# Kernel optimization log

Measured on AMD Instinct MI355X. Metric: run time of the kernel, lower is better.

The kernel has to match this reference:

```python
import jax, jax.numpy as jnp
import numpy as np

N = 25000   # total nodes across the batch of graphs
K = 16      # sample_size_per_layer
H = 128     # encoder_hidden_dim
E = 128     # embedding_size
V = 32000   # vocab size
B = 50      # number of graphs / sql sequences
L = 128     # sql sequence length
NT = 4      # tokens per node name
NLAYERS = 3 # sample_layer_size


def _nrm(k, shape):
    return jax.random.normal(k, shape, dtype=jnp.float32) * 0.05


def setup_inputs() -> dict:
    key = jax.random.key(0)
    ks = iter(jax.random.split(key, 48))
    inp = {}
    inp["embed"] = _nrm(next(ks), (V, E))
    for d in ("seq_f", "seq_b", "node"):
        inp[d + "_Wih"] = _nrm(next(ks), (4 * H, E))
        inp[d + "_Whh"] = _nrm(next(ks), (4 * H, H))
        inp[d + "_b"] = _nrm(next(ks), (4 * H,))
    for d in ("fw", "bw"):
        inp[d + "_att0"] = _nrm(next(ks), (2, H))
        inp[d + "_attr"] = _nrm(next(ks), (NLAYERS - 1, 2, 2 * H))
        inp[d + "_Wg0"] = _nrm(next(ks), (H, H))
        inp[d + "_bg0"] = _nrm(next(ks), (H,))
        inp[d + "_Wgr"] = _nrm(next(ks), (NLAYERS - 1, 2 * H, 2 * H))
        inp[d + "_bgr"] = _nrm(next(ks), (NLAYERS - 1, 2 * H))
        inp[d + "_Wo0"] = _nrm(next(ks), (2, H, H))
        inp[d + "_bo0"] = _nrm(next(ks), (2, H))
        inp[d + "_Wor"] = _nrm(next(ks), (NLAYERS - 1, 2, 2 * H, H))
        inp[d + "_bor"] = _nrm(next(ks), (NLAYERS - 1, 2, H))
    inp["node_features"] = jax.random.randint(next(ks), (N, NT), 0, V)
    inp["fw_adj"] = jax.random.randint(next(ks), (N + 1, K), 0, N + 1)  # index N = zero-pad row
    inp["bw_adj"] = jax.random.randint(next(ks), (N + 1, K), 0, N + 1)
    inp["idx_sql_seqs"] = jax.random.randint(next(ks), (B, L), 0, V)
    lens = jax.random.randint(next(ks), (B,), 16, L + 1)
    inp["sql_seqs_lens"] = lens.at[0].set(L)  # ensure max(lens) == L like pad_packed
    inp["max_len"] = 1000  # nodes per graph (equal-size graphs)
    return inp


def _lstm(x, Wih, Whh, b):
    # x: [B, T, E] -> [B, T, H]; torch LSTM gate order i, f, g, o (bih+bhh folded into b)
    xg = jnp.einsum('bte,ge->btg', x, Wih) + b
    h0 = jnp.zeros((x.shape[0], Whh.shape[1]), x.dtype)
    def step(carry, gt):
        h, c = carry
        g = gt + h @ Whh.T
        i, f, gg, o = jnp.split(g, 4, axis=-1)
        c = jax.nn.sigmoid(f) * c + jax.nn.sigmoid(i) * jnp.tanh(gg)
        h = jax.nn.sigmoid(o) * jnp.tanh(c)
        return (h, c), h
    _, hs = jax.lax.scan(step, (h0, h0), jnp.swapaxes(xg, 0, 1))
    return jnp.swapaxes(hs, 0, 1)


def _gated_attn(self_h, neigh, att, Wg, bg, Wo, bo):
    # additive attention over K sampled neighbors, gated context, concat output (2*H)
    scores = jnp.einsum('nkd,d->nk', neigh, att[1]) + (self_h @ att[0])[:, None]
    a = jax.nn.softmax(scores, axis=-1)
    ctx = jnp.einsum('nk,nkd->nd', a, neigh)
    gate = jax.nn.sigmoid(self_h @ Wg + bg)
    from_self = jax.nn.relu(self_h @ Wo[0] + bo[0])
    from_neigh = jax.nn.relu((gate * ctx) @ Wo[1] + bo[1])
    return jnp.concatenate([from_self, from_neigh], axis=-1)


def reference(embed, seq_f_Wih, seq_f_Whh, seq_f_b, seq_b_Wih, seq_b_Whh, seq_b_b,
              node_Wih, node_Whh, node_b,
              fw_att0, fw_attr, fw_Wg0, fw_bg0, fw_Wgr, fw_bgr, fw_Wo0, fw_bo0, fw_Wor, fw_bor,
              bw_att0, bw_attr, bw_Wg0, bw_bg0, bw_Wgr, bw_bgr, bw_Wo0, bw_bo0, bw_Wor, bw_bor,
              node_features, fw_adj, bw_adj, idx_sql_seqs, sql_seqs_lens, max_len):
    Bq, Lq = idx_sql_seqs.shape
    # --- SQL sequence encoder: bi-LSTM with length-aware reverse (pack/pad semantics) ---
    se = embed[idx_sql_seqs]                              # [B, L, E]
    fwd = _lstm(se, seq_f_Wih, seq_f_Whh, seq_f_b)
    rev_idx = jnp.clip(sql_seqs_lens[:, None] - 1 - jnp.arange(Lq)[None, :], 0, Lq - 1)
    se_rev = jnp.take_along_axis(se, rev_idx[..., None], 1)
    bwd = jnp.take_along_axis(_lstm(se_rev, seq_b_Wih, seq_b_Whh, seq_b_b), rev_idx[..., None], 1)
    valid = (jnp.arange(Lq)[None, :] < sql_seqs_lens[:, None])[..., None]
    seqs_encoding = jnp.concatenate([fwd, bwd], -1) * valid  # padded positions zeroed
    seqs_encoding_mask = (idx_sql_seqs == 0)
    # --- node feature encoder: last hidden of a uni-LSTM over node tokens ---
    node_embedding = _lstm(embed[node_features], node_Wih, node_Whh, node_b)[:, -1, :]  # [N, H]
    fw_nbrs = fw_adj[:-1]  # [N, K]
    bw_nbrs = bw_adj[:-1]
    fw_hidden = node_embedding
    bw_hidden = node_embedding
    for l in range(NLAYERS):
        pad = jnp.zeros((1, fw_hidden.shape[1]), fw_hidden.dtype)
        fn = jnp.concatenate([fw_hidden, pad], 0)[fw_nbrs]  # [N, K, d]
        if l == 0:
            fw_hidden = _gated_attn(fw_hidden, fn, fw_att0, fw_Wg0, fw_bg0, fw_Wo0, fw_bo0)
        else:
            j = l - 1
            fw_hidden = _gated_attn(fw_hidden, fn, fw_attr[j], fw_Wgr[j], fw_bgr[j], fw_Wor[j], fw_bor[j])
        bn_ = jnp.concatenate([bw_hidden, pad], 0)[bw_nbrs]
        if l == 0:
            bw_hidden = _gated_attn(bw_hidden, bn_, bw_att0, bw_Wg0, bw_bg0, bw_Wo0, bw_bo0)
        else:
            j = l - 1
            bw_hidden = _gated_attn(bw_hidden, bn_, bw_attr[j], bw_Wgr[j], bw_bgr[j], bw_Wor[j], bw_bor[j])
    hidden = jax.nn.relu(jnp.concatenate([fw_hidden, bw_hidden], -1))  # [N, 4H]
    graph_hidden = hidden.reshape(hidden.shape[0] // max_len, max_len, hidden.shape[1])
    graph_embedding = graph_hidden.max(axis=1)
    return (graph_hidden, graph_embedding, max_len, seqs_encoding, seqs_encoding_mask)
```

## Files before the change

### kernel.cpp

```cpp
#include <hip/hip_runtime.h>
#include <math.h>

#define NN 25000
#define KNB 16
#define HH 128
#define VV 32000
#define BB 50
#define LL 128
#define NTK 4
#define NGRAPH 25
#define GCH 20

typedef __attribute__((ext_vector_type(8))) short s16x8;
typedef __attribute__((ext_vector_type(4))) float f32x4;
typedef _Float16 h16x2 __attribute__((ext_vector_type(2)));

__device__ __forceinline__ float fexp2(float x) {
#if __has_builtin(__builtin_amdgcn_exp2f)
    return __builtin_amdgcn_exp2f(x);
#else
    return exp2f(x);
#endif
}
__device__ __forceinline__ float frcp(float x) {
#if __has_builtin(__builtin_amdgcn_rcpf)
    return __builtin_amdgcn_rcpf(x);
#else
    return 1.f / x;
#endif
}
__device__ __forceinline__ float fsigm(float x) { return frcp(1.f + fexp2(x * -1.4426950408889634f)); }
__device__ __forceinline__ float ftanh(float x) { return 1.f - 2.f * frcp(1.f + fexp2(x * 2.8853900817779268f)); }

__device__ __forceinline__ unsigned short f2bf(float x) {
    unsigned int u = __float_as_uint(x);
    unsigned int r = (u + 0x7fffu + ((u >> 16) & 1u)) >> 16;
    return (unsigned short)r;
}
__device__ __forceinline__ float bf2f(unsigned int b) {
    return __uint_as_float((b & 0xffffu) << 16);
}

template<int CTRL>
__device__ __forceinline__ float qxor(float x) {
#if __has_builtin(__builtin_amdgcn_mov_dpp)
    return __int_as_float(__builtin_amdgcn_mov_dpp(__float_as_int(x), CTRL, 0xf, 0xf, true));
#else
    int m = (CTRL == 0xB1) ? 1 : (CTRL == 0x4E) ? 2 : 3;
    return __shfl_xor(x, m, 64);
#endif
}

__device__ __forceinline__ float hdot(unsigned int a, unsigned int b, float c) {
#if __has_builtin(__builtin_amdgcn_fdot2)
    return __builtin_amdgcn_fdot2(__builtin_bit_cast(h16x2, a), __builtin_bit_cast(h16x2, b), c, false);
#else
    h16x2 av = __builtin_bit_cast(h16x2, a), bv = __builtin_bit_cast(h16x2, b);
    return c + (float)av[0] * (float)bv[0] + (float)av[1] * (float)bv[1];
#endif
}

__global__ __launch_bounds__(256) void embconv_k(const float* __restrict__ e,
                                                 unsigned short* __restrict__ o)
{
    int i = blockIdx.x * 256 + threadIdx.x;
    if (i < VV * 128) o[i] = f2bf(e[i]);
}

__global__ __launch_bounds__(256) void wprep_k(
    const float* __restrict__ ndWih, const float* __restrict__ ndWhh,
    const float* __restrict__ fWg0, const float* __restrict__ fWgr,
    const float* __restrict__ fWo0, const float* __restrict__ fWor,
    const float* __restrict__ bWg0, const float* __restrict__ bWgr,
    const float* __restrict__ bWo0, const float* __restrict__ bWor,
    const float* __restrict__ sfWih, const float* __restrict__ sbWih,
    const float* __restrict__ sfWhh, const float* __restrict__ sbWhh,
    unsigned short* __restrict__ dst)
{
    int idx = blockIdx.x * 256 + threadIdx.x;
    if (idx >= 1146880) return;
    if (idx >= 884736) {
        int r = idx - 884736;
        int d = r >> 17;
        int o = r & 131071;
        int pairIdx = o >> 1, hf = o & 1;
        int k2 = pairIdx >> 9, n = pairIdx & 511;
        int k = k2 * 2 + hf;
        int unit = n >> 2, gate = n & 3;
        const float* W = d ? sbWhh : sfWhh;
        _Float16 hv = (_Float16)W[(gate * 128 + unit) * 128 + k];
        dst[idx] = __builtin_bit_cast(unsigned short, hv);
        return;
    }
    float val;
    if (idx < 131072) {
        int r = idx >> 8, k = idx & 255;
        int unit = r >> 2, gate = r & 3;
        int srow = (gate << 7) + unit;
        val = (k < 128) ? ndWih[srow * 128 + k] : ndWhh[srow * 128 + (k - 128)];
    } else if (idx < 753664) {
        int r = idx - 131072;
        int dir = r / 311296;
        int o = r % 311296;
        const float* Wg0 = dir ? bWg0 : fWg0;
        const float* Wgr = dir ? bWgr : fWgr;
        const float* Wo0 = dir ? bWo0 : fWo0;
        const float* Wor = dir ? bWor : fWor;
        if (o < 16384) {
            int n = o >> 7, k = o & 127;
            val = Wg0[k * 128 + n];
        } else if (o < 147456) {
            int p = o - 16384;
            int j = p >> 16, q = p & 65535;
            int n = q >> 8, k = q & 255;
            val = Wgr[j * 65536 + k * 256 + n];
        } else if (o < 180224) {
            int p = o - 147456;
            int s = p >> 14, q = p & 16383;
            int n = q >> 7, k = q & 127;
            val = Wo0[s * 16384 + k * 128 + n];
        } else {
            int p = o - 180224;
            int js = p >> 15, q = p & 32767;
            int n = q >> 8, k = q & 255;
            val = Wor[js * 32768 + k * 128 + n];
        }
    } else if (idx < 819200) {
        val = sfWih[idx - 753664];
    } else {
        val = sbWih[idx - 819200];
    }
    dst[idx] = f2bf(val);
}

__global__ __launch_bounds__(256) void tokrev_k(const int* __restrict__ idx,
                                                const int* __restrict__ lens,
                                                int* __restrict__ tokrev)
{
    int t = blockIdx.x * 256 + threadIdx.x;
    if (t >= BB * LL) return;
    int b = t / LL, tt = t % LL;
    int r = lens[b] - 1 - tt;
    r = r < 0 ? 0 : (r > LL - 1 ? LL - 1 : r);
    tokrev[t] = idx[b * LL + r];
}

__global__ __launch_bounds__(256) void hgemm1_k(
    const unsigned short* __restrict__ embedbf,
    const int* __restrict__ gidxA, const int* __restrict__ gidxB,
    const unsigned short* __restrict__ WtA, const unsigned short* __restrict__ WtB,
    const float* __restrict__ biasA, const float* __restrict__ biasB,
    float* __restrict__ outA, float* __restrict__ outB)
{
    __shared__ unsigned short Asm[128 * 64];
    __shared__ unsigned short Bsm[128 * 64];
    const int tid = threadIdx.x;
    const int lane = tid & 63, w = tid >> 6;
    const int wm = w >> 1, wn = w & 1;
    const int lane15 = lane & 15, hi = lane >> 4;
    const int y = blockIdx.y;
    const int* gidx = (y < 4) ? gidxA : gidxB;
    const unsigned short* Wt = (y < 4) ? WtA : WtB;
    const float* bias = (y < 4) ? biasA : biasB;
    float* outp = (y < 4) ? outA : outB;
    const int bm0 = blockIdx.x * 128, bn0 = (y & 3) * 128;
    const int M = BB * LL, K = 128;
    f32x4 acc[4][4];
#pragma unroll
    for (int i = 0; i < 4; ++i)
#pragma unroll
        for (int j = 0; j < 4; ++j) acc[i][j] = (f32x4){0.f, 0.f, 0.f, 0.f};

    for (int kt = 0; kt < K; kt += 64) {
#pragma unroll
        for (int r = 0; r < 4; ++r) {
            int id = tid + r * 256;
            int row = id >> 3, cc = id & 7;
            int m = bm0 + row;
            s16x8 v = {0, 0, 0, 0, 0, 0, 0, 0};
            if (m < M) {
                int g = gidx[m];
                v = *(const s16x8*)(embedbf + (size_t)g * 128 + kt + cc * 8);
            }
            int byt = (cc * 16) ^ ((row & 7) << 4);
            *(s16x8*)((char*)Asm + row * 128 + byt) = v;
        }
#pragma unroll
        for (int r = 0; r < 4; ++r) {
            int id = tid + r * 256;
            int row = id >> 3, cc = id & 7;
            s16x8 v = *(const s16x8*)(Wt + (size_t)(bn0 + row) * K + kt + cc * 8);
            int byt = (cc * 16) ^ ((row & 7) << 4);
            *(s16x8*)((char*)Bsm + row * 128 + byt) = v;
        }
        __syncthreads();
#pragma unroll
        for (int ks = 0; ks < 2; ++ks) {
            s16x8 af[4], bf[4];
#pragma unroll
            for (int mi = 0; mi < 4; ++mi) {
                int row = wm * 64 + mi * 16 + lane15;
                int byt = (ks * 64 + (hi * 16)) ^ ((row & 7) << 4);
                af[mi] = *(const s16x8*)((char*)Asm + row * 128 + byt);
            }
#pragma unroll
            for (int ni = 0; ni < 4; ++ni) {
                int row = wn * 64 + ni * 16 + lane15;
                int byt = (ks * 64 + (hi * 16)) ^ ((row & 7) << 4);
                bf[ni] = *(const s16x8*)((char*)Bsm + row * 128 + byt);
            }
#pragma unroll
            for (int mi = 0; mi < 4; ++mi)
#pragma unroll
                for (int ni = 0; ni < 4; ++ni)
                    acc[mi][ni] = __builtin_amdgcn_mfma_f32_16x16x32_bf16(af[mi], bf[ni], acc[mi][ni], 0, 0, 0);
        }
        __syncthreads();
    }
#pragma unroll
    for (int mi = 0; mi < 4; ++mi) {
#pragma unroll
        for (int ni = 0; ni < 4; ++ni) {
            int n = bn0 + wn * 64 + ni * 16 + lane15;
#pragma unroll
            for (int j = 0; j < 4; ++j) {
                int m = bm0 + wm * 64 + mi * 16 + hi * 4 + j;
                if (m < M) {
                    float v = acc[mi][ni][j] + bias[n];
                    int nn = ((n & 127) << 2) | (n >> 7);
                    outp[(size_t)m * 512 + nn] = v;
                }
            }
        }
    }
}

__global__ __launch_bounds__(512, 4) void node_seq_k(
    const unsigned short* __restrict__ embedbf,
    const int* __restrict__ nodefeat,
    const unsigned short* __restrict__ hrd,
    const unsigned short* __restrict__ nodeW,
    const float* __restrict__ ndb,
    unsigned short* __restrict__ hwr,
    unsigned short* __restrict__ cbuf,
    int step,
    const float* __restrict__ xgf, const float* __restrict__ xgb,
    const unsigned short* __restrict__ wseq,
    const int* __restrict__ lens,
    float* __restrict__ senc,
    unsigned short* __restrict__ hseq, float* __restrict__ cseq)
{
    __shared__ __align__(16) unsigned char smem[32768 + 512];
    const int bid = blockIdx.x;
    const int tid = threadIdx.x;

    if (bid >= 784) {
        int sid = bid - 784;
        int dir = sid >= BB ? 1 : 0;
        int b = dir ? sid - BB : sid;
        int len = lens[b];
        int t0 = step * 32;
        if (t0 >= len) return;
        int t1 = t0 + 32 < len ? t0 + 32 : len;
        const float* xg = (dir ? xgb : xgf) + (size_t)b * LL * 512;
        const unsigned int* wp = (const unsigned int*)(wseq + dir * 131072);
        int q = tid & 3, unit = tid >> 2;
        unsigned int wreg[64];
#pragma unroll
        for (int k2 = 0; k2 < 64; ++k2) wreg[k2] = wp[k2 * 512 + tid];
        unsigned short* hlsq = (unsigned short*)smem;
        float cj = 0.f;
        if (step == 0) {
            if (tid < 128) hlsq[tid] = 0;
        } else {
            if (tid < 128) hlsq[tid] = hseq[sid * 128 + tid];
            if (q == 0) cj = cseq[sid * 128 + unit];
        }
        __syncthreads();
        float xcur = xg[(size_t)t0 * 512 + tid];
        int pb = 0;
        for (int t = t0; t < t1; ++t) {
            float xnext = (t + 1 < t1) ? xg[(size_t)(t + 1) * 512 + tid] : 0.f;
            const uint4* hp = (const uint4*)&hlsq[pb * 128];
            float p0 = 0.f, p1 = 0.f, p2 = 0.f, p3 = 0.f;
#pragma unroll
            for (int i = 0; i < 4; ++i) {
                uint4 h0 = hp[i * 4 + 0], h1 = hp[i * 4 + 1], h2 = hp[i * 4 + 2], h3 = hp[i * 4 + 3];
                const unsigned int* w0 = &wreg[i * 16];
                p0 = hdot(h0.x, w0[0], p0);  p0 = hdot(h0.y, w0[1], p0);
                p0 = hdot(h0.z, w0[2], p0);  p0 = hdot(h0.w, w0[3], p0);
                p1 = hdot(h1.x, w0[4], p1);  p1 = hdot(h1.y, w0[5], p1);
                p1 = hdot(h1.z, w0[6], p1);  p1 = hdot(h1.w, w0[7], p1);
                p2 = hdot(h2.x, w0[8], p2);  p2 = hdot(h2.y, w0[9], p2);
                p2 = hdot(h2.z, w0[10], p2); p2 = hdot(h2.w, w0[11], p2);
                p3 = hdot(h3.x, w0[12], p3); p3 = hdot(h3.y, w0[13], p3);
                p3 = hdot(h3.z, w0[14], p3); p3 = hdot(h3.w, w0[15], p3);
            }
            float accv = xcur + ((p0 + p1) + (p2 + p3));
            float tv = (q == 2) ? ftanh(accv) : fsigm(accv);
            float v1 = __shfl_xor(tv, 1), v2 = __shfl_xor(tv, 2), v3 = __shfl_xor(tv, 3);
            if (q == 0) {
                cj = v1 * cj + tv * v2;
                float hv = v3 * ftanh(cj);
                _Float16 hh = (_Float16)hv;
                hlsq[(pb ^ 1) * 128 + unit] = __builtin_bit_cast(unsigned short, hh);
                int tout = dir ? (len - 1 - t) : t;
                senc[((size_t)b * LL + tout) * 256 + dir * 128 + unit] = hv;
            }
            __syncthreads();
            pb ^= 1;
            xcur = xnext;
        }
        if (q == 0) cseq[sid * 128 + unit] = cj;
        if (tid < 128) hseq[sid * 128 + tid] = hlsq[pb * 128 + tid];
        return;
    }

    unsigned short* Asm = (unsigned short*)smem;
    unsigned short* Bsm = (unsigned short*)(smem + 16384);
    const int lane = tid & 63, w = tid >> 6;
    const int wm = w & 1, wn = w >> 1;
    const int lane15 = lane & 15, hi = lane >> 4, q = lane & 3;
    const int bx = bid % 196, y = bid / 196;
    const int bm0 = bx * 128, bn0 = y * 128;
    const int czero = (step == 0);

    f32x4 acc[4][2];
#pragma unroll
    for (int i = 0; i < 4; ++i)
#pragma unroll
        for (int j = 0; j < 2; ++j) acc[i][j] = (f32x4){0.f, 0.f, 0.f, 0.f};

    for (int kt = 0; kt < 256; kt += 64) {
#pragma unroll
        for (int r = 0; r < 2; ++r) {
            int id = tid + r * 512;
            int row = id >> 3, cc = id & 7;
            int m = bm0 + row;
            s16x8 v = {0, 0, 0, 0, 0, 0, 0, 0};
            if (m < NN) {
                int k0 = kt + cc * 8;
                if (k0 < 128) {
                    int g = nodefeat[m * NTK + step];
                    v = *(const s16x8*)(embedbf + (size_t)g * 128 + k0);
                } else if (!czero) {
                    v = *(const s16x8*)(hrd + (size_t)m * 128 + (k0 - 128));
                }
            }
            int byt = (cc * 16) ^ ((row & 7) << 4);
            *(s16x8*)((char*)Asm + row * 128 + byt) = v;
        }
#pragma unroll
        for (int r = 0; r < 2; ++r) {
            int id = tid + r * 512;
            int row = id >> 3, cc = id & 7;
            s16x8 v = *(const s16x8*)(nodeW + (size_t)(bn0 + row) * 256 + kt + cc * 8);
            int byt = (cc * 16) ^ ((row & 7) << 4);
            *(s16x8*)((char*)Bsm + row * 128 + byt) = v;
        }
        __syncthreads();
#pragma unroll
        for (int ks = 0; ks < 2; ++ks) {
            s16x8 af[4], bf[2];
#pragma unroll
            for (int mi = 0; mi < 4; ++mi) {
                int row = wm * 64 + mi * 16 + lane15;
                int byt = (ks * 64 + (hi * 16)) ^ ((row & 7) << 4);
                af[mi] = *(const s16x8*)((char*)Asm + row * 128 + byt);
            }
#pragma unroll
            for (int ni = 0; ni < 2; ++ni) {
                int row = wn * 32 + ni * 16 + lane15;
                int byt = (ks * 64 + (hi * 16)) ^ ((row & 7) << 4);
                bf[ni] = *(const s16x8*)((char*)Bsm + row * 128 + byt);
            }
#pragma unroll
            for (int mi = 0; mi < 4; ++mi)
#pragma unroll
                for (int ni = 0; ni < 2; ++ni)
                    acc[mi][ni] = __builtin_amdgcn_mfma_f32_16x16x32_bf16(af[mi], bf[ni], acc[mi][ni], 0, 0, 0);
        }
        __syncthreads();
    }
    unsigned short* cb = cbuf + (((size_t)bid * 8 + w) * 64 + lane) * 8;
    float crv[8];
    if (czero) {
#pragma unroll
        for (int i = 0; i < 8; ++i) crv[i] = 0.f;
    } else {
        uint4 w0 = *(const uint4*)cb;
        unsigned int wd[4] = {w0.x, w0.y, w0.z, w0.w};
#pragma unroll
        for (int i = 0; i < 8; ++i) crv[i] = bf2f(wd[i >> 1] >> ((i & 1) * 16));
    }
    const bool qb0 = (lane & 1), qb1 = (lane & 2);
#pragma unroll
    for (int mi = 0; mi < 4; ++mi) {
#pragma unroll
        for (int ni = 0; ni < 2; ++ni) {
            int n = bn0 + wn * 32 + ni * 16 + lane15;
            int unit = n >> 2;
            float bval = ndb[((n & 3) << 7) + unit];
#pragma unroll
            for (int j = 0; j < 4; ++j) {
                float v = acc[mi][ni][j] + bval;
                float tv = (q == 2) ? ftanh(v) : fsigm(v);
                float v1 = qxor<0xB1>(tv), v2 = qxor<0x4E>(tv), v3 = qxor<0x1B>(tv);
                if (q == j) {
                    float gf = qb0 ? (qb1 ? v2 : tv) : (qb1 ? v3 : v1);
                    float gig = qb0 ? (v1 * v3) : (tv * v2);
                    float go = qb0 ? (qb1 ? tv : v2) : (qb1 ? v1 : v3);
                    float cc = gf * crv[mi * 2 + ni] + gig;
                    crv[mi * 2 + ni] = cc;
                    int m = bm0 + wm * 64 + mi * 16 + hi * 4 + j;
                    if (m < NN) hwr[(size_t)m * HH + unit] = f2bf(go * ftanh(cc));
                }
            }
        }
    }
    unsigned int wd[4];
#pragma unroll
    for (int p = 0; p < 4; ++p)
        wd[p] = (unsigned int)f2bf(crv[2 * p]) | ((unsigned int)f2bf(crv[2 * p + 1]) << 16);
    *(uint4*)cb = make_uint4(wd[0], wd[1], wd[2], wd[3]);
}

template<int D, int OF32OUT>
__global__ __launch_bounds__(512, 1) void layer_fused_k(
    const unsigned short* __restrict__ cur, int curds,
    const unsigned short* __restrict__ ctx, int ctxds,
    const unsigned short* __restrict__ wg, int wgds,
    const float* __restrict__ bgf, const float* __restrict__ bgb,
    const unsigned short* __restrict__ wo, int wods, int wrs,
    const float* __restrict__ bof, const float* __restrict__ bob,
    void* __restrict__ outb, int outds)
{
    __shared__ unsigned short As[128 * D];
    __shared__ unsigned short Gs[128 * D];
    __shared__ unsigned short Ws[128 * 64];
    constexpr int gt = D / 128;
    const int tid = threadIdx.x;
    const int lane = tid & 63, w = tid >> 6;
    const int wm = w & 1, wn = w >> 1;
    const int lane15 = lane & 15, hi = lane >> 4;
    const int orig = blockIdx.x;
    const int work = (orig & 7) * 49 + (orig >> 3);
    const int dir = work / 196;
    const int mt = work % 196;
    const int bm0 = mt * 128;
    const unsigned short* curd = cur + (size_t)dir * curds;
    const unsigned short* ctxd = ctx + (size_t)dir * ctxds;
    const float* bg = dir ? bgb : bgf;
    const float* bo = dir ? bob : bof;

    constexpr int CH = D / 8;
#pragma unroll
    for (int r = 0; r < D / 32; ++r) {
        int id = tid + r * 512;
        int row = id / CH, cc = id % CH;
        int m = bm0 + row;
        s16x8 v = {0, 0, 0, 0, 0, 0, 0, 0};
        if (m < NN) v = *(const s16x8*)(curd + (size_t)m * D + cc * 8);
        *(s16x8*)((char*)As + row * (D * 2) + ((cc * 16) ^ ((row & 7) << 4))) = v;
    }
    __syncthreads();

#pragma unroll
    for (int p = 0; p <= gt; ++p) {
        const bool isgate = p < gt;
        const int colBase = isgate ? p * 128 : 0;
        const unsigned short* Wt = isgate ? (wg + (size_t)dir * wgds + (size_t)colBase * D)
                                          : (wo + (size_t)dir * wods);
        f32x4 acc[4][2];
#pragma unroll
        for (int i = 0; i < 4; ++i)
#pragma unroll
            for (int j = 0; j < 2; ++j) acc[i][j] = (f32x4){0.f, 0.f, 0.f, 0.f};
        for (int kt = 0; kt < D; kt += 64) {
#pragma unroll
            for (int r = 0; r < 2; ++r) {
                int id = tid + r * 512;
                int row = id >> 3, cc = id & 7;
                s16x8 v = *(const s16x8*)(Wt + (size_t)row * D + kt + cc * 8);
                *(s16x8*)((char*)Ws + row * 128 + ((cc * 16) ^ ((row & 7) << 4))) = v;
            }
            __syncthreads();
#pragma unroll
            for (int ks = 0; ks < 2; ++ks) {
                s16x8 af[4], bf[2];
#pragma unroll
                for (int mi = 0; mi < 4; ++mi) {
                    int row = wm * 64 + mi * 16 + lane15;
                    af[mi] = *(const s16x8*)((char*)As + row * (D * 2)
                              + (((kt + ks * 32 + hi * 8) * 2) ^ ((row & 7) << 4)));
                }
#pragma unroll
                for (int ni = 0; ni < 2; ++ni) {
                    int row = wn * 32 + ni * 16 + lane15;
                    bf[ni] = *(const s16x8*)((char*)Ws + row * 128
                              + (((ks * 32 + hi * 8) * 2) ^ ((row & 7) << 4)));
                }
#pragma unroll
                for (int mi = 0; mi < 4; ++mi)
#pragma unroll
                    for (int ni = 0; ni < 2; ++ni)
                        acc[mi][ni] = __builtin_amdgcn_mfma_f32_16x16x32_bf16(af[mi], bf[ni], acc[mi][ni], 0, 0, 0);
            }
            __syncthreads();
        }
#pragma unroll
        for (int mi = 0; mi < 4; ++mi) {
#pragma unroll
            for (int ni = 0; ni < 2; ++ni) {
                int ncol = wn * 32 + ni * 16 + lane15;
#pragma unroll
                for (int j = 0; j < 4; ++j) {
                    int rr = wm * 64 + mi * 16 + hi * 4 + j;
                    int m = bm0 + rr;
                    if (isgate) {
                        int col = colBase + ncol;
                        float v = acc[mi][ni][j] + bg[col];
                        int ma = (m < NN) ? m : 0;
                        v = fsigm(v) * bf2f(ctxd[(size_t)ma * D + col]);
                        *(unsigned short*)((char*)Gs + rr * (D * 2) + ((col * 2) ^ ((rr & 7) << 4))) = f2bf(v);
                    } else if (m < NN) {
                        float v = fmaxf(acc[mi][ni][j] + bo[ncol], 0.f);
                        if (OF32OUT) ((float*)outb)[(size_t)m * 512 + dir * 256 + ncol] = v;
                        else ((unsigned short*)outb)[(size_t)dir * outds + (size_t)m * 256 + ncol] = f2bf(v);
                    }
                }
            }
        }
    }
    __syncthreads();

    {
        const unsigned short* Wt = wo + (size_t)dir * wods + (size_t)wrs;
        f32x4 acc[4][2];
#pragma unroll
        for (int i = 0; i < 4; ++i)
#pragma unroll
            for (int j = 0; j < 2; ++j) acc[i][j] = (f32x4){0.f, 0.f, 0.f, 0.f};
        for (int kt = 0; kt < D; kt += 64) {
#pragma unroll
            for (int r = 0; r < 2; ++r) {
                int id = tid + r * 512;
                int row = id >> 3, cc = id & 7;
                s16x8 v = *(const s16x8*)(Wt + (size_t)row * D + kt + cc * 8);
                *(s16x8*)((char*)Ws + row * 128 + ((cc * 16) ^ ((row & 7) << 4))) = v;
            }
            __syncthreads();
#pragma unroll
            for (int ks = 0; ks < 2; ++ks) {
                s16x8 af[4], bf[2];
#pragma unroll
                for (int mi = 0; mi < 4; ++mi) {
                    int row = wm * 64 + mi * 16 + lane15;
                    af[mi] = *(const s16x8*)((char*)Gs + row * (D * 2)
                              + (((kt + ks * 32 + hi * 8) * 2) ^ ((row & 7) << 4)));
                }
#pragma unroll
                for (int ni = 0; ni < 2; ++ni) {
                    int row = wn * 32 + ni * 16 + lane15;
                    bf[ni] = *(const s16x8*)((char*)Ws + row * 128
                              + (((ks * 32 + hi * 8) * 2) ^ ((row & 7) << 4)));
                }
#pragma unroll
                for (int mi = 0; mi < 4; ++mi)
#pragma unroll
                    for (int ni = 0; ni < 2; ++ni)
                        acc[mi][ni] = __builtin_amdgcn_mfma_f32_16x16x32_bf16(af[mi], bf[ni], acc[mi][ni], 0, 0, 0);
            }
            __syncthreads();
        }
#pragma unroll
        for (int mi = 0; mi < 4; ++mi) {
#pragma unroll
            for (int ni = 0; ni < 2; ++ni) {
                int ncol = wn * 32 + ni * 16 + lane15;
#pragma unroll
                for (int j = 0; j < 4; ++j) {
                    int m = bm0 + wm * 64 + mi * 16 + hi * 4 + j;
                    if (m < NN) {
                        float v = fmaxf(acc[mi][ni][j] + bo[128 + ncol], 0.f);
                        if (OF32OUT) ((float*)outb)[(size_t)m * 512 + dir * 256 + 128 + ncol] = v;
                        else ((unsigned short*)outb)[(size_t)dir * outds + (size_t)m * 256 + 128 + ncol] = f2bf(v);
                    }
                }
            }
        }
    }
}

__global__ __launch_bounds__(256) void finalize_k(const int* __restrict__ idx,
                                                  const int* __restrict__ lens,
                                                  float* __restrict__ senc,
                                                  float* __restrict__ mask,
                                                  float* __restrict__ omax,
                                                  const int* __restrict__ mlin)
{
    int id = blockIdx.x * 256 + threadIdx.x;
    if (id == 0) omax[0] = (float)mlin[0];
    if (id >= BB * LL * 64) return;
    int row = id >> 6, c = id & 63;
    int b = row / LL, tt = row % LL;
    if (c == 0) mask[row] = (idx[row] == 0) ? 1.f : 0.f;
    if (tt >= lens[b]) *(float4*)&senc[(size_t)row * 256 + c * 4] = make_float4(0.f, 0.f, 0.f, 0.f);
}

template<int D>
__global__ __launch_bounds__(256) void sdot_k(const unsigned short* __restrict__ hidb, int hidds,
                                              const float* __restrict__ a1f, const float* __restrict__ a1b,
                                              float* __restrict__ s1)
{
    constexpr int V = D / 64;
    int dir = blockIdx.y;
    const unsigned short* hid = hidb + (size_t)dir * hidds;
    const float* att1 = dir ? a1b : a1f;
    int lane = threadIdx.x & 63, wid = threadIdx.x >> 6;
    int n = blockIdx.x * 4 + wid;
    if (n >= NN) return;
    float p = 0.f;
    if (V == 2) {
        unsigned int u = *(const unsigned int*)(hid + (size_t)n * D + lane * 2);
        p = bf2f(u) * att1[lane * 2] + bf2f(u >> 16) * att1[lane * 2 + 1];
    } else {
        uint2 u = *(const uint2*)(hid + (size_t)n * D + lane * 4);
        p = bf2f(u.x) * att1[lane * 4] + bf2f(u.x >> 16) * att1[lane * 4 + 1]
          + bf2f(u.y) * att1[lane * 4 + 2] + bf2f(u.y >> 16) * att1[lane * 4 + 3];
    }
#pragma unroll
    for (int m = 1; m < 64; m <<= 1) p += __shfl_xor(p, m);
    if (lane == 0) s1[dir * NN + n] = p;
}

template<int D>
__global__ __launch_bounds__(256) void attn_ctx3_k(const unsigned short* __restrict__ hidb, int hidds,
                                                   const int* __restrict__ adj0, const int* __restrict__ adj1,
                                                   const float* __restrict__ s1,
                                                   unsigned short* __restrict__ ctxb, int ctxds)
{
    constexpr int V = D / 64;
    int dir = blockIdx.y;
    const unsigned short* hid = hidb + (size_t)dir * hidds;
    const int* adj = dir ? adj1 : adj0;
    unsigned short* ctx = ctxb + (size_t)dir * ctxds;
    int lane = threadIdx.x & 63, wid = threadIdx.x >> 6;
    int n = blockIdx.x * 4 + wid;
    if (n >= NN) return;
    int nb[KNB];
    float sc[KNB];
#pragma unroll
    for (int k = 0; k < KNB; ++k) nb[k] = adj[n * KNB + k];
#pragma unroll
    for (int k = 0; k < KNB; ++k) sc[k] = (nb[k] < NN) ? s1[dir * NN + nb[k]] : 0.f;
    float mx = sc[0];
#pragma unroll
    for (int k = 1; k < KNB; ++k) mx = fmaxf(mx, sc[k]);
    float s = 0.f;
#pragma unroll
    for (int k = 0; k < KNB; ++k) { sc[k] = fexp2((sc[k] - mx) * 1.4426950408889634f); s += sc[k]; }
    float inv = frcp(s);
    float accv[V];
#pragma unroll
    for (int j = 0; j < V; ++j) accv[j] = 0.f;
#pragma unroll
    for (int k = 0; k < KNB; ++k) {
        if (nb[k] < NN) {
            if (V == 2) {
                unsigned int u = *(const unsigned int*)(hid + (size_t)nb[k] * D + lane * 2);
                accv[0] += sc[k] * bf2f(u);
                accv[1] += sc[k] * bf2f(u >> 16);
            } else {
                uint2 u = *(const uint2*)(hid + (size_t)nb[k] * D + lane * 4);
                accv[0] += sc[k] * bf2f(u.x);
                accv[1] += sc[k] * bf2f(u.x >> 16);
                accv[2] += sc[k] * bf2f(u.y);
                accv[3] += sc[k] * bf2f(u.y >> 16);
            }
        }
    }
#pragma unroll
    for (int j2 = 0; j2 < V; j2 += 2) {
        unsigned int pk = (unsigned int)f2bf(accv[j2] * inv) | ((unsigned int)f2bf(accv[j2 + 1] * inv) << 16);
        *(unsigned int*)(ctx + (size_t)n * D + lane * V + j2) = pk;
    }
}

__global__ __launch_bounds__(512) void gmax1_k(const float* __restrict__ gh, float* __restrict__ part)
{
    int g = blockIdx.x, ch = blockIdx.y;
    int c = threadIdx.x;
    const float* p = gh + ((size_t)g * 1000 + ch * (1000 / GCH)) * 512 + c;
    float m = -1e30f;
#pragma unroll 5
    for (int i = 0; i < 1000 / GCH; ++i) m = fmaxf(m, p[(size_t)i * 512]);
    part[((size_t)g * GCH + ch) * 512 + c] = m;
}

__global__ __launch_bounds__(512) void gmax2_k(const float* __restrict__ part, float* __restrict__ ge)
{
    int g = blockIdx.x;
    int c = threadIdx.x;
    float m = -1e30f;
#pragma unroll
    for (int i = 0; i < GCH; ++i) m = fmaxf(m, part[((size_t)g * GCH + i) * 512 + c]);
    ge[g * 512 + c] = m;
}

extern "C" void kernel_launch(void* const* d_in, const int* in_sizes, int n_in,
                              void* d_out, int out_size, void* d_ws, size_t ws_size,
                              hipStream_t stream)
{
    const float* embed = (const float*)d_in[0];
    const float* sfWhh = (const float*)d_in[2];
    const float* sfb   = (const float*)d_in[3];
    const float* sbWhh = (const float*)d_in[5];
    const float* sbb   = (const float*)d_in[6];
    const float* ndWih = (const float*)d_in[7];
    const float* ndWhh = (const float*)d_in[8];
    const float* ndb   = (const float*)d_in[9];
    const int* nodefeat = (const int*)d_in[30];
    const int* adj0     = (const int*)d_in[31];
    const int* adj1     = (const int*)d_in[32];
    const int* idxseq   = (const int*)d_in[33];
    const int* lens     = (const int*)d_in[34];
    const int* mlin     = (const int*)d_in[35];

    float* ws = (float*)d_ws;
    unsigned short* warena  = (unsigned short*)ws;
    unsigned short* embedbf = (unsigned short*)(ws + 573440);
    float* xgf = ws + 2621440;
    float* xgb = ws + 5898240;
    int*   tokrev = (int*)(ws + 9175040);
    unsigned short* hbf  = (unsigned short*)(ws + 9181440);
    unsigned short* hbf2 = (unsigned short*)(ws + 10781440);
    unsigned short* cbuf = (unsigned short*)(ws + 12381440);
    unsigned short* HA   = (unsigned short*)(ws + 573440);
    unsigned short* HB   = (unsigned short*)(ws + 6973440);
    unsigned short* ctxb = (unsigned short*)(ws + 13987072);
    float* s1buf = ws + 20387072;
    unsigned short* hseq = (unsigned short*)(ws + 20437072);
    float* cseq = ws + 20449872;
    float* gmaxp = ws + 573440;

    float* outf  = (float*)d_out;
    float* gh    = outf;
    float* ge    = outf + 12800000;
    float* omax  = outf + 12812800;
    float* senc  = outf + 12812801;
    float* omask = outf + 14451201;

    tokrev_k<<<dim3((BB * LL + 255) / 256), dim3(256), 0, stream>>>(idxseq, lens, tokrev);
    embconv_k<<<dim3(VV * 128 / 256), dim3(256), 0, stream>>>(embed, embedbf);
    wprep_k<<<dim3(4480), dim3(256), 0, stream>>>(ndWih, ndWhh,
        (const float*)d_in[12], (const float*)d_in[14], (const float*)d_in[16], (const float*)d_in[18],
        (const float*)d_in[22], (const float*)d_in[24], (const float*)d_in[26], (const float*)d_in[28],
        (const float*)d_in[1], (const float*)d_in[4], sfWhh, sbWhh, warena);

    hgemm1_k<<<dim3(50, 8), dim3(256), 0, stream>>>(embedbf, idxseq, tokrev,
        warena + 753664, warena + 819200, sfb, sbb, xgf, xgb);

    for (int t = 0; t < NTK; ++t) {
        const unsigned short* hrd = (t & 1) ? hbf2 : hbf;
        unsigned short* hwr = (t & 1) ? hbf : hbf2;
        node_seq_k<<<dim3(884), dim3(512), 0, stream>>>(embedbf, nodefeat, hrd,
            warena, ndb, hwr, cbuf, t,
            xgf, xgb, warena + 884736, lens, senc, hseq, cseq);
    }
    finalize_k<<<dim3(1600), dim3(256), 0, stream>>>(idxseq, lens, senc, omask, omax, mlin);

    for (int l = 0; l < 3; ++l) {
        int D = (l == 0) ? 128 : 256;
        int j = l - 1;
        const unsigned short* curb = (l == 0) ? hbf : (l == 1 ? HA : HB);
        int curds = (l == 0) ? 0 : NN * 256;
        int ctxds = NN * D;
        const float* a1f = (l == 0) ? (const float*)d_in[10] + 128 : (const float*)d_in[11] + (size_t)j * 512 + 256;
        const float* a1b = (l == 0) ? (const float*)d_in[20] + 128 : (const float*)d_in[21] + (size_t)j * 512 + 256;

        if (D == 128) {
            sdot_k<128><<<dim3(NN / 4, 2), dim3(256), 0, stream>>>(curb, curds, a1f, a1b, s1buf);
            attn_ctx3_k<128><<<dim3(NN / 4, 2), dim3(256), 0, stream>>>(curb, curds, adj0, adj1, s1buf, ctxb, ctxds);
        } else {
            sdot_k<256><<<dim3(NN / 4, 2), dim3(256), 0, stream>>>(curb, curds, a1f, a1b, s1buf);
            attn_ctx3_k<256><<<dim3(NN / 4, 2), dim3(256), 0, stream>>>(curb, curds, adj0, adj1, s1buf, ctxb, ctxds);
        }

        const unsigned short* wgb = warena + 131072 + ((l == 0) ? 0 : 16384 + j * 65536);
        const float* bgf = (l == 0) ? (const float*)d_in[13] : (const float*)d_in[15] + (size_t)j * 256;
        const float* bgb = (l == 0) ? (const float*)d_in[23] : (const float*)d_in[25] + (size_t)j * 256;
        const unsigned short* wob = warena + 131072 + ((l == 0) ? 147456 : 180224 + j * 65536);
        int wrs = (l == 0) ? 16384 : 32768;
        const float* bof = (l == 0) ? (const float*)d_in[17] : (const float*)d_in[19] + (size_t)j * 256;
        const float* bob = (l == 0) ? (const float*)d_in[27] : (const float*)d_in[29] + (size_t)j * 256;
        int outds = NN * 256;

        if (l == 0) {
            layer_fused_k<128, 0><<<dim3(392), dim3(512), 0, stream>>>(curb, curds, ctxb, ctxds,
                wgb, 311296, bgf, bgb, wob, 311296, wrs, bof, bob, HA, outds);
        } else if (l == 1) {
            layer_fused_k<256, 0><<<dim3(392), dim3(512), 0, stream>>>(curb, curds, ctxb, ctxds,
                wgb, 311296, bgf, bgb, wob, 311296, wrs, bof, bob, HB, outds);
        } else {
            layer_fused_k<256, 1><<<dim3(392), dim3(512), 0, stream>>>(curb, curds, ctxb, ctxds,
                wgb, 311296, bgf, bgb, wob, 311296, wrs, bof, bob, gh, 0);
        }
    }

    gmax1_k<<<dim3(NGRAPH, GCH), dim3(512), 0, stream>>>(gh, gmaxp);
    gmax2_k<<<dim3(NGRAPH), dim3(512), 0, stream>>>(gmaxp, ge);
}
```

Before: 606.2 us.

## Halve layer GEMM row tile to 64 and double blocks for occupancy

The fused gated-attention layer kernel now processes 64 rows per block instead of 128, halving its shared-memory footprint and doubling the grid to 784 blocks, with launch bounds raised to allow two blocks per CU. Each wave now computes a 16x64 output strip (one A fragment, four B fragments) instead of 64x32. The gate results are packed in pairs via lane shuffles into 32-bit LDS writes. This aims to improve occupancy and load balance across CUs, but weight tiles are reloaded twice as often per output row and each A fragment is reused less.

```diff
diff --git a/kernel.cpp b/kernel.cpp
--- a/kernel.cpp
+++ b/kernel.cpp
@@ -426,7 +426,7 @@
 }
 
 template<int D, int OF32OUT>
-__global__ __launch_bounds__(512, 1) void layer_fused_k(
+__global__ __launch_bounds__(512, 2) void layer_fused_k(
     const unsigned short* __restrict__ cur, int curds,
     const unsigned short* __restrict__ ctx, int ctxds,
     const unsigned short* __restrict__ wg, int wgds,
@@ -435,19 +435,19 @@
     const float* __restrict__ bof, const float* __restrict__ bob,
     void* __restrict__ outb, int outds)
 {
-    __shared__ unsigned short As[128 * D];
-    __shared__ unsigned short Gs[128 * D];
+    __shared__ unsigned short As[64 * D];
+    __shared__ unsigned short Gs[64 * D];
     __shared__ unsigned short Ws[128 * 64];
     constexpr int gt = D / 128;
     const int tid = threadIdx.x;
     const int lane = tid & 63, w = tid >> 6;
-    const int wm = w & 1, wn = w >> 1;
+    const int wm = w >> 1, wn = w & 1;
     const int lane15 = lane & 15, hi = lane >> 4;
     const int orig = blockIdx.x;
-    const int work = (orig & 7) * 49 + (orig >> 3);
-    const int dir = work / 196;
-    const int mt = work % 196;
-    const int bm0 = mt * 128;
+    const int work = (orig & 7) * 98 + (orig >> 3);
+    const int dir = work / 392;
+    const int mt = work % 392;
+    const int bm0 = mt * 64;
     const unsigned short* curd = cur + (size_t)dir * curds;
     const unsigned short* ctxd = ctx + (size_t)dir * ctxds;
     const float* bg = dir ? bgb : bgf;
@@ -455,7 +455,7 @@
 
     constexpr int CH = D / 8;
 #pragma unroll
-    for (int r = 0; r < D / 32; ++r) {
+    for (int r = 0; r < D / 64; ++r) {
         int id = tid + r * 512;
         int row = id / CH, cc = id % CH;
         int m = bm0 + row;
@@ -471,11 +471,9 @@
         const int colBase = isgate ? p * 128 : 0;
         const unsigned short* Wt = isgate ? (wg + (size_t)dir * wgds + (size_t)colBase * D)
                                           : (wo + (size_t)dir * wods);
-        f32x4 acc[4][2];
-#pragma unroll
-        for (int i = 0; i < 4; ++i)
-#pragma unroll
-            for (int j = 0; j < 2; ++j) acc[i][j] = (f32x4){0.f, 0.f, 0.f, 0.f};
+        f32x4 acc[4];
+#pragma unroll
+        for (int i = 0; i < 4; ++i) acc[i] = (f32x4){0.f, 0.f, 0.f, 0.f};
         for (int kt = 0; kt < D; kt += 64) {
 #pragma unroll
             for (int r = 0; r < 2; ++r) {
@@ -487,47 +485,44 @@
             __syncthreads();
 #pragma unroll
             for (int ks = 0; ks < 2; ++ks) {
-                s16x8 af[4], bf[2];
-#pragma unroll
-                for (int mi = 0; mi < 4; ++mi) {
-                    int row = wm * 64 + mi * 16 + lane15;
-                    af[mi] = *(const s16x8*)((char*)As + row * (D * 2)
+                s16x8 af;
+                {
+                    int row = wm * 16 + lane15;
+                    af = *(const s16x8*)((char*)As + row * (D * 2)
                               + (((kt + ks * 32 + hi * 8) * 2) ^ ((row & 7) << 4)));
                 }
 #pragma unroll
-                for (int ni = 0; ni < 2; ++ni) {
-                    int row = wn * 32 + ni * 16 + lane15;
-                    bf[ni] = *(const s16x8*)((char*)Ws + row * 128
+                for (int ni = 0; ni < 4; ++ni) {
+                    int row = wn * 64 + ni * 16 + lane15;
+                    s16x8 bf = *(const s16x8*)((char*)Ws + row * 128
                               + (((ks * 32 + hi * 8) * 2) ^ ((row & 7) << 4)));
-                }
-#pragma unroll
-                for (int mi = 0; mi < 4; ++mi)
-#pragma unroll
-                    for (int ni = 0; ni < 2; ++ni)
-                        acc[mi][ni] = __builtin_amdgcn_mfma_f32_16x16x32_bf16(af[mi], bf[ni], acc[mi][ni], 0, 0, 0);
+                    acc[ni] = __builtin_amdgcn_mfma_f32_16x16x32_bf16(af, bf, acc[ni], 0, 0, 0);
+                }
             }
             __syncthreads();
         }
 #pragma unroll
-        for (int mi = 0; mi < 4; ++mi) {
-#pragma unroll
-            for (int ni = 0; ni < 2; ++ni) {
-                int ncol = wn * 32 + ni * 16 + lane15;
-#pragma unroll
-                for (int j = 0; j < 4; ++j) {
-                    int rr = wm * 64 + mi * 16 + hi * 4 + j;
-                    int m = bm0 + rr;
-                    if (isgate) {
-                        int col = colBase + ncol;
-                        float v = acc[mi][ni][j] + bg[col];
-                        int ma = (m < NN) ? m : 0;
-                        v = fsigm(v) * bf2f(ctxd[(size_t)ma * D + col]);
-                        *(unsigned short*)((char*)Gs + rr * (D * 2) + ((col * 2) ^ ((rr & 7) << 4))) = f2bf(v);
-                    } else if (m < NN) {
-                        float v = fmaxf(acc[mi][ni][j] + bo[ncol], 0.f);
-                        if (OF32OUT) ((float*)outb)[(size_t)m * 512 + dir * 256 + ncol] = v;
-                        else ((unsigned short*)outb)[(size_t)dir * outds + (size_t)m * 256 + ncol] = f2bf(v);
+        for (int ni = 0; ni < 4; ++ni) {
+            int ncol = wn * 64 + ni * 16 + lane15;
+#pragma unroll
+            for (int j = 0; j < 4; ++j) {
+                int rr = wm * 16 + hi * 4 + j;
+                int m = bm0 + rr;
+                if (isgate) {
+                    int col = colBase + ncol;
+                    float v = acc[ni][j] + bg[col];
+                    int ma = (m < NN) ? m : 0;
+                    v = fsigm(v) * bf2f(ctxd[(size_t)ma * D + col]);
+                    unsigned int pv = f2bf(v);
+                    unsigned int po = __shfl_xor((int)pv, 1);
+                    if ((lane15 & 1) == 0) {
+                        unsigned int word = pv | (po << 16);
+                        *(unsigned int*)((char*)Gs + rr * (D * 2) + (((col * 2) & ~3) ^ ((rr & 7) << 4))) = word;
                     }
+                } else if (m < NN) {
+                    float v = fmaxf(acc[ni][j] + bo[ncol], 0.f);
+                    if (OF32OUT) ((float*)outb)[(size_t)m * 512 + dir * 256 + ncol] = v;
+                    else ((unsigned short*)outb)[(size_t)dir * outds + (size_t)m * 256 + ncol] = f2bf(v);
                 }
             }
         }
@@ -536,11 +531,9 @@
 
     {
         const unsigned short* Wt = wo + (size_t)dir * wods + (size_t)wrs;
-        f32x4 acc[4][2];
-#pragma unroll
-        for (int i = 0; i < 4; ++i)
-#pragma unroll
-            for (int j = 0; j < 2; ++j) acc[i][j] = (f32x4){0.f, 0.f, 0.f, 0.f};
+        f32x4 acc[4];
+#pragma unroll
+        for (int i = 0; i < 4; ++i) acc[i] = (f32x4){0.f, 0.f, 0.f, 0.f};
         for (int kt = 0; kt < D; kt += 64) {
 #pragma unroll
             for (int r = 0; r < 2; ++r) {
@@ -552,40 +545,32 @@
             __syncthreads();
 #pragma unroll
             for (int ks = 0; ks < 2; ++ks) {
-                s16x8 af[4], bf[2];
-#pragma unroll
-                for (int mi = 0; mi < 4; ++mi) {
-                    int row = wm * 64 + mi * 16 + lane15;
-                    af[mi] = *(const s16x8*)((char*)Gs + row * (D * 2)
+                s16x8 af;
+                {
+                    int row = wm * 16 + lane15;
+                    af = *(const s16x8*)((char*)Gs + row * (D * 2)
                               + (((kt + ks * 32 + hi * 8) * 2) ^ ((row & 7) << 4)));
                 }
 #pragma unroll
-                for (int ni = 0; ni < 2; ++ni) {
-                    int row = wn * 32 + ni * 16 + lane15;
-                    bf[ni] = *(const s16x8*)((char*)Ws + row * 128
+                for (int ni = 0; ni < 4; ++ni) {
+                    int row = wn * 64 + ni * 16 + lane15;
+                    s16x8 bf = *(const s16x8*)((char*)Ws + row * 128
                               + (((ks * 32 + hi * 8) * 2) ^ ((row & 7) << 4)));
-                }
-#pragma unroll
-                for (int mi = 0; mi < 4; ++mi)
-#pragma unroll
-                    for (int ni = 0; ni < 2; ++ni)
-                        acc[mi][ni] = __builtin_amdgcn_mfma_f32_16x16x32_bf16(af[mi], bf[ni], acc[mi][ni], 0, 0, 0);
+                    acc[ni] = __builtin_amdgcn_mfma_f32_16x16x32_bf16(af, bf, acc[ni], 0, 0, 0);
+                }
             }
             __syncthreads();
         }
 #pragma unroll
-        for (int mi = 0; mi < 4; ++mi) {
-#pragma unroll
-            for (int ni = 0; ni < 2; ++ni) {
-                int ncol = wn * 32 + ni * 16 + lane15;
-#pragma unroll
-                for (int j = 0; j < 4; ++j) {
-                    int m = bm0 + wm * 64 + mi * 16 + hi * 4 + j;
-                    if (m < NN) {
-                        float v = fmaxf(acc[mi][ni][j] + bo[128 + ncol], 0.f);
-                        if (OF32OUT) ((float*)outb)[(size_t)m * 512 + dir * 256 + 128 + ncol] = v;
-                        else ((unsigned short*)outb)[(size_t)dir * outds + (size_t)m * 256 + 128 + ncol] = f2bf(v);
-                    }
+        for (int ni = 0; ni < 4; ++ni) {
+            int ncol = wn * 64 + ni * 16 + lane15;
+#pragma unroll
+            for (int j = 0; j < 4; ++j) {
+                int m = bm0 + wm * 16 + hi * 4 + j;
+                if (m < NN) {
+                    float v = fmaxf(acc[ni][j] + bo[128 + ncol], 0.f);
+                    if (OF32OUT) ((float*)outb)[(size_t)m * 512 + dir * 256 + 128 + ncol] = v;
+                    else ((unsigned short*)outb)[(size_t)dir * outds + (size_t)m * 256 + 128 + ncol] = f2bf(v);
                 }
             }
         }
@@ -797,13 +782,13 @@
         int outds = NN * 256;
 
         if (l == 0) {
-            layer_fused_k<128, 0><<<dim3(392), dim3(512), 0, stream>>>(curb, curds, ctxb, ctxds,
+            layer_fused_k<128, 0><<<dim3(784), dim3(512), 0, stream>>>(curb, curds, ctxb, ctxds,
                 wgb, 311296, bgf, bgb, wob, 311296, wrs, bof, bob, HA, outds);
         } else if (l == 1) {
-            layer_fused_k<256, 0><<<dim3(392), dim3(512), 0, stream>>>(curb, curds, ctxb, ctxds,
+            layer_fused_k<256, 0><<<dim3(784), dim3(512), 0, stream>>>(curb, curds, ctxb, ctxds,
                 wgb, 311296, bgf, bgb, wob, 311296, wrs, bof, bob, HB, outds);
         } else {
-            layer_fused_k<256, 1><<<dim3(392), dim3(512), 0, stream>>>(curb, curds, ctxb, ctxds,
+            layer_fused_k<256, 1><<<dim3(784), dim3(512), 0, stream>>>(curb, curds, ctxb, ctxds,
                 wgb, 311296, bgf, bgb, wob, 311296, wrs, bof, bob, gh, 0);
         }
     }
```

Measured after the change: 563.9 us. 7.0% less time.
